# Optimization experiments

Measured on AMD Instinct MI355X. Metric: run time of the kernel, lower is better.

## Reference

```python
import jax, jax.numpy as jnp
import numpy as np

EMBED_DIM = 1024
NUM_HEADS = 16


def setup_inputs() -> dict:
    key = jax.random.key(0)
    kx, kq, kk, kv, ko = jax.random.split(key, 5)
    B, S, D = 2, 2048, EMBED_DIM
    s = 1.0 / np.sqrt(D)
    return {
        "x": jax.random.normal(kx, (B, S, D), dtype=jnp.float32),
        "Wq": jax.random.normal(kq, (D, D), dtype=jnp.float32) * s,
        "Wk": jax.random.normal(kk, (D, D), dtype=jnp.float32) * s,
        "Wv": jax.random.normal(kv, (D, D), dtype=jnp.float32) * s,
        "Wo": jax.random.normal(ko, (D, D), dtype=jnp.float32) * s,
    }


def reference(x, Wq, Wk, Wv, Wo):
    B, S, D = x.shape
    H = NUM_HEADS
    d_k = D // H
    # QKV projections (nn.Linear applies x @ W.T)
    q = (x @ Wq.T).reshape(B, S, H, d_k).transpose(0, 2, 1, 3)  # [B,H,S,d_k]
    k = (x @ Wk.T).reshape(B, S, H, d_k).transpose(0, 2, 1, 3)
    v = (x @ Wv.T).reshape(B, S, H, d_k).transpose(0, 2, 1, 3)
    scores = jnp.einsum("bhqd,bhkd->bhqk", q, k) / jnp.sqrt(jnp.float32(d_k))
    probs = jax.nn.softmax(scores, axis=-1)  # dropout is identity in eval
    attn = jnp.einsum("bhqk,bhkd->bhqd", probs, v)  # [B,H,S,d_k]
    attn = attn.transpose(0, 2, 1, 3).reshape(B, S, D)
    return attn @ Wo.T
```

## Files before the change

kernel.cpp:

```cpp
#include <hip/hip_runtime.h>
#include <stdint.h>

typedef __attribute__((ext_vector_type(4))) float    f32x4;
typedef __attribute__((ext_vector_type(8))) _Float16 half8;
typedef __attribute__((ext_vector_type(4))) _Float16 half4;
typedef unsigned long long u64;

#define MFMA16(a, b, c)    __builtin_amdgcn_mfma_f32_16x16x32_f16(a, b, c, 0, 0, 0)
#define MFMA16K16(a, b, c) __builtin_amdgcn_mfma_f32_16x16x16f16(a, b, c, 0, 0, 0)

#if __has_builtin(__builtin_amdgcn_exp2f)
#define EXP2F(x) __builtin_amdgcn_exp2f(x)
#else
#define EXP2F(x) exp2f(x)
#endif

#define CEXP 0.18033688f

__device__ inline void gl_lds16(const void* g, void* l) {
    __builtin_amdgcn_global_load_lds(
        (const __attribute__((address_space(1))) unsigned int*)g,
        (__attribute__((address_space(3))) unsigned int*)l, 16, 0, 0);
}

__global__ __launch_bounds__(256) void cast_all(
    const float* __restrict__ x,  const float* __restrict__ wq,
    const float* __restrict__ wk, const float* __restrict__ wv,
    const float* __restrict__ wo,
    _Float16* __restrict__ xh,  _Float16* __restrict__ wqh,
    _Float16* __restrict__ wkh, _Float16* __restrict__ wvh,
    _Float16* __restrict__ woh) {
    const int NX = 4194304, NW = 1048576;
    int i = (blockIdx.x * 256 + threadIdx.x) * 4;
    const float* src; _Float16* dst; int off;
    if (i < NX) { src = x; dst = xh; off = i; }
    else {
        int j = i - NX; int w = j >> 20; off = j & (NW - 1);
        src = (w == 0) ? wq : (w == 1) ? wk : (w == 2) ? wv : wo;
        dst = (w == 0) ? wqh : (w == 1) ? wkh : (w == 2) ? wvh : woh;
    }
    f32x4 v = *(const f32x4*)(src + off);
    half4 o;
    o.x = (_Float16)v.x; o.y = (_Float16)v.y; o.z = (_Float16)v.z; o.w = (_Float16)v.w;
    *(half4*)(dst + off) = o;
}

#define BN 128
#define BK 64

template <int MODE>
__global__ __launch_bounds__(256) void gemm_bt(const _Float16* __restrict__ A,
                                               const _Float16* __restrict__ B,
                                               void* __restrict__ C0,
                                               void* __restrict__ C1,
                                               void* __restrict__ C2,
                                               int M, int N, int K) {
    constexpr int BM  = (MODE == 3) ? 128 : 64;
    constexpr int MT  = BM / 32;
    constexpr int AIT = BM / 32;

    __shared__ __attribute__((aligned(16))) _Float16 smem[(BM + BN) * BK];
    _Float16* As = smem;
    _Float16* Bs = smem + BM * BK;

    const int tid  = threadIdx.x;
    const int wave = tid >> 6;
    const int lane = tid & 63;
    const int l16  = lane & 15;
    const int quad = lane >> 4;
    const int m0 = blockIdx.y * BM;
    const int n0 = blockIdx.x * BN;
    const int wm = (wave >> 1) * (BM / 2);
    const int wn = (wave & 1) * 64;

    const int srow = tid >> 3;
    const int scc  = (tid & 7) ^ ((tid >> 3) & 7);

    f32x4 acc[MT][4];
#pragma unroll
    for (int i = 0; i < MT; i++)
#pragma unroll
        for (int j = 0; j < 4; j++) acc[i][j] = (f32x4){0.f, 0.f, 0.f, 0.f};

    for (int k0 = 0; k0 < K; k0 += BK) {
        __syncthreads();
#pragma unroll
        for (int i = 0; i < AIT; i++)
            gl_lds16(A + (size_t)(m0 + i * 32 + srow) * K + k0 + scc * 8,
                     (char*)As + i * 4096 + wave * 1024);
#pragma unroll
        for (int i = 0; i < 4; i++)
            gl_lds16(B + (size_t)(n0 + i * 32 + srow) * K + k0 + scc * 8,
                     (char*)Bs + i * 4096 + wave * 1024);
        __syncthreads();

#pragma unroll
        for (int kk = 0; kk < 2; kk++) {
            half8 af[MT], bf[4];
#pragma unroll
            for (int mt = 0; mt < MT; mt++) {
                int row = wm + mt * 16 + l16;
                af[mt] = *(const half8*)(As + row * 64 + ((quad + 4 * kk) ^ (row & 7)) * 8);
            }
#pragma unroll
            for (int nt = 0; nt < 4; nt++) {
                int row = wn + nt * 16 + l16;
                bf[nt] = *(const half8*)(Bs + row * 64 + ((quad + 4 * kk) ^ (row & 7)) * 8);
            }
#pragma unroll
            for (int mt = 0; mt < MT; mt++)
#pragma unroll
                for (int nt = 0; nt < 4; nt++)
                    acc[mt][nt] = MFMA16(af[mt], bf[nt], acc[mt][nt]);
        }
    }

    if (MODE == 0) {
        float* C = (float*)C0;
#pragma unroll
        for (int mt = 0; mt < MT; mt++)
#pragma unroll
            for (int r = 0; r < 4; r++) {
                int row = m0 + wm + mt * 16 + quad * 4 + r;
                float* Crow = C + (size_t)row * N + n0 + wn + l16;
#pragma unroll
                for (int nt = 0; nt < 4; nt++) Crow[nt * 16] = acc[mt][nt][r];
            }
    } else {
        const int region = n0 >> 10;
        const int nb = (n0 & 1023) + wn;
        if (region < 2) {
            _Float16* C = (region == 0) ? (_Float16*)C0 : (_Float16*)C1;
            const float scale = (region == 0) ? CEXP : 1.f;
#pragma unroll
            for (int mt = 0; mt < MT; mt++)
#pragma unroll
                for (int r = 0; r < 4; r++) {
                    int mg = m0 + wm + mt * 16 + quad * 4 + r;
                    int b = mg >> 11, s = mg & 2047;
#pragma unroll
                    for (int nt = 0; nt < 4; nt++) {
                        int nw = nb + nt * 16 + l16;
                        int h = nw >> 6, d = nw & 63;
                        C[(((size_t)b * 16 + h) * 2048 + s) * 64 + d] =
                            (_Float16)(acc[mt][nt][r] * scale);
                    }
                }
        } else {
            __syncthreads();
            _Float16* ep = smem + wave * 4096;
#pragma unroll
            for (int mt = 0; mt < MT; mt++)
#pragma unroll
                for (int nt = 0; nt < 4; nt++) {
                    int dn = nt * 16 + l16;
                    int slot = (mt * 2 + (quad >> 1)) ^ (dn & 7);
                    union { half4 h; u64 q; } o;
#pragma unroll
                    for (int r = 0; r < 4; r++) o.h[r] = (_Float16)acc[mt][nt][r];
                    *(u64*)(ep + dn * 64 + slot * 8 + (quad & 1) * 4) = o.q;
                }
            __syncthreads();
            int mgb = m0 + wm;
            int b = mgb >> 11, sbase = mgb & 2047;
            int h = nb >> 6;
            _Float16* C = (_Float16*)C2 + ((size_t)b * 16 + h) * 64 * 2048;
#pragma unroll
            for (int j = 0; j < 8; j++) {
                int dn = j * 8 + (lane >> 3);
                int slot = (lane & 7) ^ (dn & 7);
                half8 val = *(const half8*)(ep + dn * 64 + slot * 8);
                *(half8*)(C + (size_t)dn * 2048 + sbase + (lane & 7) * 8) = val;
            }
        }
    }
}

__global__ __launch_bounds__(512, 4) void attn_kernel(const _Float16* __restrict__ Q,
                                                      const _Float16* __restrict__ Kg,
                                                      const _Float16* __restrict__ Vt,
                                                      _Float16* __restrict__ Oa) {
    __shared__ __attribute__((aligned(16))) _Float16 smem[20480];

    const int tid  = threadIdx.x;
    const int wave = tid >> 6;
    const int lane = tid & 63;
    const int l16  = lane & 15;
    const int quad = lane >> 4;
    const int qw   = wave & 3;
    const int kg   = wave >> 2;
    const int bh = blockIdx.y;
    const int q0 = blockIdx.x * 128 + qw * 32;

    _Float16* Ksw = smem + kg * 4096;
    _Float16* Vsw = smem + 8192 + kg * 4096;

    half8 qf[2][2];
#pragma unroll
    for (int qt = 0; qt < 2; qt++)
#pragma unroll
        for (int kk = 0; kk < 2; kk++)
            qf[qt][kk] = *(const half8*)(Q + ((size_t)bh * 2048 + q0 + qt * 16 + l16) * 64 +
                                         (quad + 4 * kk) * 8);

    const int srow = tid >> 3;
    const int sc8  = tid & 7;
    const int kslot = sc8 ^ (srow & 7);

    const _Float16* kp = Kg + (size_t)bh * 2048 * 64 + (size_t)srow * 64 + sc8 * 8;
    const _Float16* vp = Vt + (size_t)bh * 64 * 2048 + (size_t)srow * 2048 + sc8 * 8;

    f32x4 lsum4[2];
    f32x4 oacc[2][4];
#pragma unroll
    for (int qt = 0; qt < 2; qt++) {
        lsum4[qt] = (f32x4){0.f, 0.f, 0.f, 0.f};
#pragma unroll
        for (int dt = 0; dt < 4; dt++) oacc[qt][dt] = (f32x4){0.f, 0.f, 0.f, 0.f};
    }

    half8 kr0 = *(const half8*)(kp);
    half8 kr1 = *(const half8*)(kp + 64 * 64);
    half8 vr0 = *(const half8*)(vp);
    half8 vr1 = *(const half8*)(vp + 64);

    for (int it = 0; it < 16; it++) {
        __syncthreads();
        *(half8*)(smem + srow * 64 + kslot * 8) = kr0;
        *(half8*)(smem + 4096 + srow * 64 + kslot * 8) = kr1;
        *(half8*)(smem + 8192 + srow * 64 + kslot * 8) = vr0;
        *(half8*)(smem + 12288 + srow * 64 + kslot * 8) = vr1;
        __syncthreads();

        {
            int ktp2 = ((it + 1) & 15) * 128;
            kr0 = *(const half8*)(kp + (size_t)ktp2 * 64);
            kr1 = *(const half8*)(kp + (size_t)(ktp2 + 64) * 64);
            vr0 = *(const half8*)(vp + ktp2);
            vr1 = *(const half8*)(vp + ktp2 + 64);
        }

        f32x4 sc4[2][4];
#pragma unroll
        for (int nt = 0; nt < 4; nt++) {
            int row = nt * 16 + l16;
            half8 kf0 = *(const half8*)(Ksw + row * 64 + (quad ^ (row & 7)) * 8);
            half8 kf1 = *(const half8*)(Ksw + row * 64 + ((quad + 4) ^ (row & 7)) * 8);
#pragma unroll
            for (int qt = 0; qt < 2; qt++) {
                f32x4 s = (f32x4){0.f, 0.f, 0.f, 0.f};
                s = MFMA16(kf0, qf[qt][0], s);
                s = MFMA16(kf1, qf[qt][1], s);
                sc4[qt][nt] = s;
            }
        }

        half4 ph[2][4];
#pragma unroll
        for (int qt = 0; qt < 2; qt++)
#pragma unroll
            for (int nt = 0; nt < 4; nt++) {
                half4 p;
#pragma unroll
                for (int r = 0; r < 4; r++) {
                    float pe = EXP2F(sc4[qt][nt][r]);
                    lsum4[qt][r] += pe;
                    p[r] = (_Float16)pe;
                }
                ph[qt][nt] = p;
            }

#pragma unroll
        for (int nt = 0; nt < 4; nt++) {
#pragma unroll
            for (int dt = 0; dt < 4; dt++) {
                int row = dt * 16 + l16;
                int ch  = (nt * 2 + (quad >> 1)) ^ (row & 7);
                half4 vf = *(const half4*)(Vsw + row * 64 + ch * 8 + (quad & 1) * 4);
#pragma unroll
                for (int qt = 0; qt < 2; qt++)
                    oacc[qt][dt] = MFMA16K16(vf, ph[qt][nt], oacc[qt][dt]);
            }
        }
    }

    __syncthreads();
    float* rp = (float*)smem + qw * 2560;
    if (kg == 1) {
#pragma unroll
        for (int qt = 0; qt < 2; qt++)
#pragma unroll
            for (int dt = 0; dt < 4; dt++)
                *(f32x4*)(rp + ((qt * 4 + dt) * 64 + lane) * 4) = oacc[qt][dt];
        *(f32x4*)(rp + (8 * 64 + lane) * 4) = lsum4[0];
        *(f32x4*)(rp + (9 * 64 + lane) * 4) = lsum4[1];
    }
    __syncthreads();
    if (kg == 0) {
#pragma unroll
        for (int qt = 0; qt < 2; qt++)
#pragma unroll
            for (int dt = 0; dt < 4; dt++)
                oacc[qt][dt] += *(const f32x4*)(rp + ((qt * 4 + dt) * 64 + lane) * 4);
        lsum4[0] += *(const f32x4*)(rp + (8 * 64 + lane) * 4);
        lsum4[1] += *(const f32x4*)(rp + (9 * 64 + lane) * 4);

        const int b = bh >> 4, h = bh & 15;
#pragma unroll
        for (int qt = 0; qt < 2; qt++) {
            float ls = (lsum4[qt][0] + lsum4[qt][1]) + (lsum4[qt][2] + lsum4[qt][3]);
            ls += __shfl_xor(ls, 16);
            ls += __shfl_xor(ls, 32);
            float inv = 1.f / ls;
            int q = q0 + qt * 16 + l16;
            _Float16* orow = Oa + ((size_t)b * 2048 + q) * 1024 + h * 64;
#pragma unroll
            for (int dt = 0; dt < 4; dt++) {
                half4 o;
#pragma unroll
                for (int r = 0; r < 4; r++) o[r] = (_Float16)(oacc[qt][dt][r] * inv);
                *(half4*)(orow + dt * 16 + quad * 4) = o;
            }
        }
    }
}

extern "C" void kernel_launch(void* const* d_in, const int* in_sizes, int n_in,
                              void* d_out, int out_size, void* d_ws, size_t ws_size,
                              hipStream_t stream) {
    const float* x  = (const float*)d_in[0];
    const float* Wq = (const float*)d_in[1];
    const float* Wk = (const float*)d_in[2];
    const float* Wv = (const float*)d_in[3];
    const float* Wo = (const float*)d_in[4];
    float* out = (float*)d_out;

    const int NX = 2 * 2048 * 1024;
    const int NW = 1024 * 1024;

    _Float16* ws  = (_Float16*)d_ws;
    _Float16* xh  = ws;
    _Float16* wqh = xh + NX;
    _Float16* wkh = wqh + NW;
    _Float16* wvh = wkh + NW;
    _Float16* woh = wvh + NW;
    _Float16* Qb  = woh + NW;
    _Float16* Kb  = Qb + NX;
    _Float16* Vtb = Kb + NX;
    _Float16* Ab  = Vtb + NX;

    cast_all<<<8192, 256, 0, stream>>>(x, Wq, Wk, Wv, Wo, xh, wqh, wkh, wvh, woh);

    gemm_bt<3><<<dim3(3072 / 128, 4096 / 128), 256, 0, stream>>>(
        xh, wqh, Qb, Kb, Vtb, 4096, 3072, 1024);

    attn_kernel<<<dim3(16, 32), 512, 0, stream>>>(Qb, Kb, Vtb, Ab);

    gemm_bt<0><<<dim3(1024 / 128, 4096 / 64), 256, 0, stream>>>(
        Ab, woh, out, nullptr, nullptr, 4096, 1024, 1024);
}
```

Baseline: 183.1 us.

## Software-pipeline attention PV with QK, double-buffer V, remap blocks per XCD

New measurement: 178.2 us. 1.03x faster.

```diff
diff --git a/kernel.cpp b/kernel.cpp
--- a/kernel.cpp
+++ b/kernel.cpp
@@ -7,7 +7,6 @@
 typedef unsigned long long u64;
 
 #define MFMA16(a, b, c)    __builtin_amdgcn_mfma_f32_16x16x32_f16(a, b, c, 0, 0, 0)
-#define MFMA16K16(a, b, c) __builtin_amdgcn_mfma_f32_16x16x16f16(a, b, c, 0, 0, 0)
 
 #if __has_builtin(__builtin_amdgcn_exp2f)
 #define EXP2F(x) __builtin_amdgcn_exp2f(x)
@@ -180,7 +179,7 @@
                                                       const _Float16* __restrict__ Kg,
                                                       const _Float16* __restrict__ Vt,
                                                       _Float16* __restrict__ Oa) {
-    __shared__ __attribute__((aligned(16))) _Float16 smem[20480];
+    __shared__ __attribute__((aligned(16))) _Float16 smem[24576];
 
     const int tid  = threadIdx.x;
     const int wave = tid >> 6;
@@ -189,11 +188,14 @@
     const int quad = lane >> 4;
     const int qw   = wave & 3;
     const int kg   = wave >> 2;
-    const int bh = blockIdx.y;
-    const int q0 = blockIdx.x * 128 + qw * 32;
+
+    const int id   = blockIdx.x;
+    const int xcd  = id & 7;
+    const int slot = id >> 3;
+    const int bh   = xcd * 4 + (slot >> 4);
+    const int q0   = (slot & 15) * 128 + qw * 32;
 
     _Float16* Ksw = smem + kg * 4096;
-    _Float16* Vsw = smem + 8192 + kg * 4096;
 
     half8 qf[2][2];
 #pragma unroll
@@ -212,26 +214,97 @@
 
     f32x4 lsum4[2];
     f32x4 oacc[2][4];
+    half4 phv[2][4];
 #pragma unroll
     for (int qt = 0; qt < 2; qt++) {
         lsum4[qt] = (f32x4){0.f, 0.f, 0.f, 0.f};
 #pragma unroll
         for (int dt = 0; dt < 4; dt++) oacc[qt][dt] = (f32x4){0.f, 0.f, 0.f, 0.f};
+    }
+
+#define QKEXP_BODY(KPTR)                                                          \
+    {                                                                             \
+        f32x4 sc4[2][4];                                                          \
+        _Pragma("unroll")                                                         \
+        for (int nt = 0; nt < 4; nt++) {                                          \
+            int row = nt * 16 + l16;                                              \
+            half8 kf0 = *(const half8*)((KPTR) + row * 64 + (quad ^ (row & 7)) * 8);      \
+            half8 kf1 = *(const half8*)((KPTR) + row * 64 + ((quad + 4) ^ (row & 7)) * 8);\
+            _Pragma("unroll")                                                     \
+            for (int qt = 0; qt < 2; qt++) {                                      \
+                f32x4 s = (f32x4){0.f, 0.f, 0.f, 0.f};                            \
+                s = MFMA16(kf0, qf[qt][0], s);                                    \
+                s = MFMA16(kf1, qf[qt][1], s);                                    \
+                sc4[qt][nt] = s;                                                  \
+            }                                                                     \
+        }                                                                         \
+        _Pragma("unroll")                                                         \
+        for (int qt = 0; qt < 2; qt++)                                            \
+            _Pragma("unroll")                                                     \
+            for (int nt = 0; nt < 4; nt++) {                                      \
+                half4 p;                                                          \
+                _Pragma("unroll")                                                 \
+                for (int r = 0; r < 4; r++) {                                     \
+                    float pe = EXP2F(sc4[qt][nt][r]);                             \
+                    lsum4[qt][r] += pe;                                           \
+                    p[r] = (_Float16)pe;                                          \
+                }                                                                 \
+                phv[qt][nt] = p;                                                  \
+            }                                                                     \
+    }
+
+#define PV_BODY(VPTR)                                                             \
+    _Pragma("unroll")                                                             \
+    for (int nt2 = 0; nt2 < 2; nt2++) {                                           \
+        half8 pf[2];                                                              \
+        _Pragma("unroll")                                                         \
+        for (int qt = 0; qt < 2; qt++) {                                          \
+            union { half8 h8; half4 h4[2]; } u;                                   \
+            u.h4[0] = phv[qt][nt2 * 2];                                           \
+            u.h4[1] = phv[qt][nt2 * 2 + 1];                                       \
+            pf[qt] = u.h8;                                                        \
+        }                                                                         \
+        _Pragma("unroll")                                                         \
+        for (int dt = 0; dt < 4; dt++) {                                          \
+            int row = dt * 16 + l16;                                              \
+            int ch0 = ((nt2 * 2) * 2 + (quad >> 1)) ^ (row & 7);                  \
+            int ch1 = ((nt2 * 2 + 1) * 2 + (quad >> 1)) ^ (row & 7);              \
+            union { half8 h8; half4 h4[2]; } a;                                   \
+            a.h4[0] = *(const half4*)((VPTR) + row * 64 + ch0 * 8 + (quad & 1) * 4);  \
+            a.h4[1] = *(const half4*)((VPTR) + row * 64 + ch1 * 8 + (quad & 1) * 4);  \
+            _Pragma("unroll")                                                     \
+            for (int qt = 0; qt < 2; qt++)                                        \
+                oacc[qt][dt] = MFMA16(a.h8, pf[qt], oacc[qt][dt]);                \
+        }                                                                         \
     }
 
     half8 kr0 = *(const half8*)(kp);
     half8 kr1 = *(const half8*)(kp + 64 * 64);
     half8 vr0 = *(const half8*)(vp);
     half8 vr1 = *(const half8*)(vp + 64);
-
-    for (int it = 0; it < 16; it++) {
+    *(half8*)(smem + srow * 64 + kslot * 8) = kr0;
+    *(half8*)(smem + 4096 + srow * 64 + kslot * 8) = kr1;
+    *(half8*)(smem + 8192 + srow * 64 + kslot * 8) = vr0;
+    *(half8*)(smem + 12288 + srow * 64 + kslot * 8) = vr1;
+    __syncthreads();
+    kr0 = *(const half8*)(kp + (size_t)128 * 64);
+    kr1 = *(const half8*)(kp + (size_t)192 * 64);
+    vr0 = *(const half8*)(vp + 128);
+    vr1 = *(const half8*)(vp + 192);
+    QKEXP_BODY(Ksw)
+
+    for (int it = 1; it < 16; it++) {
         __syncthreads();
+        const int vb = 8192 + (it & 1) * 8192;
         *(half8*)(smem + srow * 64 + kslot * 8) = kr0;
         *(half8*)(smem + 4096 + srow * 64 + kslot * 8) = kr1;
-        *(half8*)(smem + 8192 + srow * 64 + kslot * 8) = vr0;
-        *(half8*)(smem + 12288 + srow * 64 + kslot * 8) = vr1;
+        *(half8*)(smem + vb + srow * 64 + kslot * 8) = vr0;
+        *(half8*)(smem + vb + 4096 + srow * 64 + kslot * 8) = vr1;
+        {
+            const _Float16* Vprev = smem + 8192 + ((it & 1) ^ 1) * 8192 + kg * 4096;
+            PV_BODY(Vprev)
+        }
         __syncthreads();
-
         {
             int ktp2 = ((it + 1) & 15) * 128;
             kr0 = *(const half8*)(kp + (size_t)ktp2 * 64);
@@ -239,49 +312,11 @@
             vr0 = *(const half8*)(vp + ktp2);
             vr1 = *(const half8*)(vp + ktp2 + 64);
         }
-
-        f32x4 sc4[2][4];
-#pragma unroll
-        for (int nt = 0; nt < 4; nt++) {
-            int row = nt * 16 + l16;
-            half8 kf0 = *(const half8*)(Ksw + row * 64 + (quad ^ (row & 7)) * 8);
-            half8 kf1 = *(const half8*)(Ksw + row * 64 + ((quad + 4) ^ (row & 7)) * 8);
-#pragma unroll
-            for (int qt = 0; qt < 2; qt++) {
-                f32x4 s = (f32x4){0.f, 0.f, 0.f, 0.f};
-                s = MFMA16(kf0, qf[qt][0], s);
-                s = MFMA16(kf1, qf[qt][1], s);
-                sc4[qt][nt] = s;
-            }
-        }
-
-        half4 ph[2][4];
-#pragma unroll
-        for (int qt = 0; qt < 2; qt++)
-#pragma unroll
-            for (int nt = 0; nt < 4; nt++) {
-                half4 p;
-#pragma unroll
-                for (int r = 0; r < 4; r++) {
-                    float pe = EXP2F(sc4[qt][nt][r]);
-                    lsum4[qt][r] += pe;
-                    p[r] = (_Float16)pe;
-                }
-                ph[qt][nt] = p;
-            }
-
-#pragma unroll
-        for (int nt = 0; nt < 4; nt++) {
-#pragma unroll
-            for (int dt = 0; dt < 4; dt++) {
-                int row = dt * 16 + l16;
-                int ch  = (nt * 2 + (quad >> 1)) ^ (row & 7);
-                half4 vf = *(const half4*)(Vsw + row * 64 + ch * 8 + (quad & 1) * 4);
-#pragma unroll
-                for (int qt = 0; qt < 2; qt++)
-                    oacc[qt][dt] = MFMA16K16(vf, ph[qt][nt], oacc[qt][dt]);
-            }
-        }
+        QKEXP_BODY(Ksw)
+    }
+    {
+        const _Float16* Vprev = smem + 16384 + kg * 4096;
+        PV_BODY(Vprev)
     }
 
     __syncthreads();
@@ -354,7 +389,7 @@
     gemm_bt<3><<<dim3(3072 / 128, 4096 / 128), 256, 0, stream>>>(
         xh, wqh, Qb, Kb, Vtb, 4096, 3072, 1024);
 
-    attn_kernel<<<dim3(16, 32), 512, 0, stream>>>(Qb, Kb, Vtb, Ab);
+    attn_kernel<<<512, 512, 0, stream>>>(Qb, Kb, Vtb, Ab);
 
     gemm_bt<0><<<dim3(1024 / 128, 4096 / 64), 256, 0, stream>>>(
         Ab, woh, out, nullptr, nullptr, 4096, 1024, 1024);
```
